# Kernel optimization log

Measured on AMD Instinct MI355X. Metric: run time of the kernel, lower is better.

Reference implementation:

```python
import jax, jax.numpy as jnp
import numpy as np

N_NODES = 1024
FEAT = 64
NEG_BIG = -9e15

def setup_inputs() -> dict:
    key = jax.random.key(0)
    ks = jax.random.split(key, 12)
    B, S, D = 4, 16384, FEAT
    flow_features = jax.random.normal(ks[0], (B, S, D), dtype=jnp.float32)
    src_ips = jax.random.randint(ks[1], (B, S), 0, N_NODES)
    dst_ips = jax.random.randint(ks[2], (B, S), 0, N_NODES)
    flow_volumes = jax.random.uniform(ks[3], (B, S), dtype=jnp.float32) * 2000.0
    emb = jax.random.normal(ks[4], (N_NODES, D), dtype=jnp.float32) * 0.02
    We1 = jax.random.normal(ks[5], (2 * D, 32), dtype=jnp.float32) * 0.1
    be1 = jnp.zeros((32,), dtype=jnp.float32)
    We2 = jax.random.normal(ks[6], (32, 1), dtype=jnp.float32) * 0.1
    be2 = jnp.zeros((1,), dtype=jnp.float32)
    W = jax.random.normal(ks[7], (D, D), dtype=jnp.float32) * 0.1
    a1 = jax.random.normal(ks[8], (D,), dtype=jnp.float32) * 0.1
    a2 = jax.random.normal(ks[9], (D,), dtype=jnp.float32) * 0.1
    return dict(flow_features=flow_features, src_ips=src_ips, dst_ips=dst_ips,
                flow_volumes=flow_volumes, emb=emb, We1=We1, be1=be1, We2=We2,
                be2=be2, W=W, a1=a1, a2=a2)

def _forward(flow_features, flow_volumes, emb, We1, be1, We2, be2, W, a1, a2,
             src_ips, dst_ips):
    B, S, D = flow_features.shape
    N = emb.shape[0]
    # --- DynamicGraphBuilder: scatter-add flow features at dst nodes ---
    node = jax.vmap(lambda f, d: jnp.zeros((N, D), f.dtype).at[d].add(f))(
        flow_features, dst_ips)                         # (B, N, D)
    nrm = jnp.maximum(jnp.linalg.norm(node, axis=-1, keepdims=True), 1e-12)
    h = node / nrm                                      # F.normalize(p=2)
    # --- edge weights: MLP over concat(src_emb, dst_emb), scaled by volume ---
    pair = jnp.concatenate([emb[src_ips], emb[dst_ips]], axis=-1)  # (B, S, 2D)
    mid = jax.nn.relu(pair @ We1 + be1)
    ew = jax.nn.sigmoid((mid @ We2 + be2)[..., 0])      # (B, S)
    w = ew * jax.nn.sigmoid(flow_volumes / 1000.0)
    adj = jax.vmap(lambda s, d, ww: jnp.zeros((N, N), ww.dtype)
                   .at[s, d].set(ww).at[d, s].set(ww))(src_ips, dst_ips, w)
    # --- GraphAttentionLayer (decomposed e_ij = a1.Wh_i + a2.Wh_j) ---
    Wh = h @ W                                          # (B, N, D)
    f1 = Wh @ a1                                        # (B, N)
    f2 = Wh @ a2                                        # (B, N)
    e = jax.nn.leaky_relu(f1[:, :, None] + f2[:, None, :], 0.2)  # (B, N, N)
    attn = jax.nn.softmax(jnp.where(adj > 0, e, NEG_BIG), axis=-1)
    return jax.nn.elu(jnp.einsum('bij,bjd->bid', attn, Wh))       # (B, N, D)

def reference(flow_features, src_ips, dst_ips, flow_volumes, emb, We1, be1,
              We2, be2, W, a1, a2):
    return _forward(flow_features, flow_volumes, emb, We1, be1, We2, be2,
                    W, a1, a2, src_ips, dst_ips)
```

## Files before the change

kernel.cpp:

```cpp
#include <hip/hip_runtime.h>
#include <math.h>

#define BB 4
#define SS 16384
#define NN 1024
#define DD 64
#define MW 32
#define KSEG 32
#define CAPSEG 12
#define NCAP 128

__device__ __forceinline__ float wave_sum(float v) {
    #pragma unroll
    for (int off = 32; off > 0; off >>= 1) v += __shfl_xor(v, off, 64);
    return v;
}
__device__ __forceinline__ float wave_max(float v) {
    #pragma unroll
    for (int off = 32; off > 0; off >>= 1) v = fmaxf(v, __shfl_xor(v, off, 64));
    return v;
}

__global__ __launch_bounds__(512) void build_kernel(
        const int* __restrict__ src_ips, const int* __restrict__ dst_ips,
        int* __restrict__ cnt_d_seg, int* __restrict__ cnt_s_seg,
        int* __restrict__ bkt_d, int* __restrict__ bkt_s) {
    __shared__ int cd[NN], cs_[NN];
    int t = threadIdx.x;
    cd[t] = 0; cd[t + 512] = 0; cs_[t] = 0; cs_[t + 512] = 0;
    __syncthreads();
    int b = blockIdx.x >> 5, seg = blockIdx.x & 31;
    int local = (seg << 9) + t;
    int f = (b << 14) + local;
    int src = src_ips[f], dst = dst_ips[f];
    int rowbase = blockIdx.x << 10;
    int pd = atomicAdd(&cd[dst], 1);
    if (pd < CAPSEG) bkt_d[(size_t)(rowbase + dst) * CAPSEG + pd] = local | (src << 16);
    int ps = atomicAdd(&cs_[src], 1);
    if (ps < CAPSEG) bkt_s[(size_t)(rowbase + src) * CAPSEG + ps] = dst;
    __syncthreads();
    cnt_d_seg[rowbase + t]       = min(cd[t], CAPSEG);
    cnt_d_seg[rowbase + t + 512] = min(cd[t + 512], CAPSEG);
    cnt_s_seg[rowbase + t]       = min(cs_[t], CAPSEG);
    cnt_s_seg[rowbase + t + 512] = min(cs_[t + 512], CAPSEG);
}

__global__ __launch_bounds__(256) void gather_kernel(
        const float* __restrict__ ff, const int* __restrict__ cnt_d_seg,
        const int* __restrict__ cnt_s_seg, const int* __restrict__ bkt_d,
        const int* __restrict__ bkt_s, const float* __restrict__ W,
        const float* __restrict__ a1, const float* __restrict__ a2,
        float* __restrict__ Wh, float* __restrict__ f1, float* __restrict__ f2,
        int* __restrict__ nbr, int* __restrict__ cntn) {
    __shared__ float Ws[DD * DD];
    __shared__ float hs[4][DD];
    __shared__ unsigned int bm[4][MW];
    __shared__ float a1s[DD], a2s[DD];
    int t = threadIdx.x, wave = t >> 6, lane = t & 63;
    for (int i = t; i < DD * DD / 4; i += 256)
        ((float4*)Ws)[i] = ((const float4*)W)[i];
    if (t < DD) { a1s[t] = a1[t]; a2s[t] = a2[t]; }
    int row = blockIdx.x * 4 + wave;
    int b = row >> 10, i = row & (NN - 1);
    if (lane < MW) bm[wave][lane] = 0u;

    int segbase = (b << 15) + i;
    int cv_d = (lane < KSEG) ? cnt_d_seg[segbase + (lane << 10)] : 0;
    int cv_s = (lane < KSEG) ? cnt_s_seg[segbase + (lane << 10)] : 0;
    int xd = cv_d, xs = cv_s;
    #pragma unroll
    for (int off = 1; off < 64; off <<= 1) {
        int yd = __shfl_up(xd, off, 64);
        int ys = __shfl_up(xs, off, 64);
        if (lane >= off) { xd += yd; xs += ys; }
    }
    int c1 = __shfl(xd, 63, 64);
    int c2 = __shfl(xs, 63, 64);
    int bd0 = xd - cv_d, bs0 = xs - cv_s;
    int bkreg = 0, dreg = 0;
    for (int s = 0; s < KSEG; ++s) {
        int csd = __shfl(cv_d, s, 64), bd = __shfl(bd0, s, 64);
        if (lane >= bd && lane < bd + csd)
            bkreg = bkt_d[(size_t)(segbase + (s << 10)) * CAPSEG + (lane - bd)];
        int css = __shfl(cv_s, s, 64), bs = __shfl(bs0, s, 64);
        if (lane >= bs && lane < bs + css)
            dreg = bkt_s[(size_t)(segbase + (s << 10)) * CAPSEG + (lane - bs)];
    }

    int fq = lane >> 4, qi = lane & 15;
    const float* ffb = ff + (size_t)b * SS * DD;
    float4 v0 = make_float4(0.f, 0.f, 0.f, 0.f);
    float4 v1 = make_float4(0.f, 0.f, 0.f, 0.f);
    int lim = min(c1, 64);
    for (int base = 0; base < lim; base += 8) {
        int w0 = __shfl(bkreg, base + fq, 64);
        int w1 = __shfl(bkreg, base + 4 + fq, 64);
        if (base + fq < lim) {
            float4 x = ((const float4*)(ffb + (size_t)(w0 & 0xFFFF) * DD))[qi];
            v0.x += x.x; v0.y += x.y; v0.z += x.z; v0.w += x.w;
        }
        if (base + 4 + fq < lim) {
            float4 x = ((const float4*)(ffb + (size_t)(w1 & 0xFFFF) * DD))[qi];
            v1.x += x.x; v1.y += x.y; v1.z += x.z; v1.w += x.w;
        }
    }
    float4 v = make_float4(v0.x + v1.x, v0.y + v1.y, v0.z + v1.z, v0.w + v1.w);
    #pragma unroll
    for (int off = 16; off <= 32; off <<= 1) {
        v.x += __shfl_xor(v.x, off, 64);
        v.y += __shfl_xor(v.y, off, 64);
        v.z += __shfl_xor(v.z, off, 64);
        v.w += __shfl_xor(v.w, off, 64);
    }
    float ssq = (fq == 0) ? (v.x*v.x + v.y*v.y + v.z*v.z + v.w*v.w) : 0.f;
    float nrm = fmaxf(sqrtf(wave_sum(ssq)), 1e-12f);
    float inv = 1.f / nrm;
    __syncthreads();
    if (fq == 0)
        ((float4*)hs[wave])[qi] = make_float4(v.x*inv, v.y*inv, v.z*inv, v.w*inv);
    float whl = 0.f;
    #pragma unroll
    for (int k = 0; k < DD; ++k)
        whl = fmaf(hs[wave][k], Ws[k * DD + lane], whl);
    Wh[(size_t)row * DD + lane] = whl;
    float p1 = wave_sum(whl * a1s[lane]);
    float p2 = wave_sum(whl * a2s[lane]);
    if (lane == 0) { f1[row] = p1; f2[row] = p2; }

    if (lane < lim) {
        int s = (bkreg >> 16) & 0x3FF;
        atomicOr(&bm[wave][s >> 5], 1u << (s & 31));
    }
    int lim2 = min(c2, 64);
    if (lane < lim2) {
        int d = dreg & 0x3FF;
        atomicOr(&bm[wave][d >> 5], 1u << (d & 31));
    }
    unsigned int mw_ = (lane < MW) ? bm[wave][lane] : 0u;
    int pc = __popc(mw_);
    int x = pc;
    #pragma unroll
    for (int off = 1; off < 64; off <<= 1) {
        int y = __shfl_up(x, off, 64);
        if (lane >= off) x += y;
    }
    int cnt = __shfl(x, 63, 64);
    int o = x - pc;
    int* nrow = nbr + (size_t)row * NCAP;
    unsigned int bits = mw_;
    while (bits) {
        int bi = __ffs(bits) - 1; bits &= bits - 1;
        nrow[o++] = (lane << 5) + bi;
    }
    if (lane == 0) cntn[row] = cnt;
}

__global__ __launch_bounds__(256) void attn_kernel(
        const int* __restrict__ cntn, const int* __restrict__ nbr,
        const float* __restrict__ f1, const float* __restrict__ f2,
        const float* __restrict__ Wh, float* __restrict__ out) {
    __shared__ int jls[4][NCAP];
    int t = threadIdx.x, wave = t >> 6, lane = t & 63;
    int row = blockIdx.x * 4 + wave;
    int b = row >> 10;
    int fq = lane >> 4, qi = lane & 15;
    int cnt = cntn[row];
    float f1i = f1[row];
    const float* f2b = f2 + b * NN;
    const float* Whb = Wh + (size_t)(b << 10) * DD;
    const int* nrow = nbr + (size_t)row * NCAP;
    for (int k = lane; k < cnt; k += 64) jls[wave][k] = nrow[k];

    if (cnt > 0) {
        float m = -INFINITY;
        for (int k = lane; k < cnt; k += 64) {
            float e = f1i + f2b[jls[wave][k]];
            e = (e >= 0.f) ? e : 0.2f * e;
            m = fmaxf(m, e);
        }
        m = wave_max(m);
        float4 a0 = make_float4(0.f, 0.f, 0.f, 0.f);
        float4 a1v = make_float4(0.f, 0.f, 0.f, 0.f);
        float psum = 0.f;
        for (int k = fq; k < cnt; k += 8) {
            int j0 = jls[wave][k];
            float e0 = f1i + f2b[j0];
            e0 = (e0 >= 0.f) ? e0 : 0.2f * e0;
            float p0 = __expf(e0 - m);
            float4 w0 = ((const float4*)(Whb + (size_t)j0 * DD))[qi];
            a0.x = fmaf(p0, w0.x, a0.x);
            a0.y = fmaf(p0, w0.y, a0.y);
            a0.z = fmaf(p0, w0.z, a0.z);
            a0.w = fmaf(p0, w0.w, a0.w);
            psum += p0;
            int k1 = k + 4;
            if (k1 < cnt) {
                int j1 = jls[wave][k1];
                float e1 = f1i + f2b[j1];
                e1 = (e1 >= 0.f) ? e1 : 0.2f * e1;
                float p1 = __expf(e1 - m);
                float4 w1 = ((const float4*)(Whb + (size_t)j1 * DD))[qi];
                a1v.x = fmaf(p1, w1.x, a1v.x);
                a1v.y = fmaf(p1, w1.y, a1v.y);
                a1v.z = fmaf(p1, w1.z, a1v.z);
                a1v.w = fmaf(p1, w1.w, a1v.w);
                psum += p1;
            }
        }
        float4 acc = make_float4(a0.x + a1v.x, a0.y + a1v.y,
                                 a0.z + a1v.z, a0.w + a1v.w);
        #pragma unroll
        for (int off = 16; off <= 32; off <<= 1) {
            acc.x += __shfl_xor(acc.x, off, 64);
            acc.y += __shfl_xor(acc.y, off, 64);
            acc.z += __shfl_xor(acc.z, off, 64);
            acc.w += __shfl_xor(acc.w, off, 64);
        }
        float lsum = wave_sum(psum) * (1.f / 16.f);
        if (fq == 0) {
            float invl = 1.f / lsum;
            float4 r;
            r.x = acc.x * invl; r.y = acc.y * invl;
            r.z = acc.z * invl; r.w = acc.w * invl;
            r.x = (r.x > 0.f) ? r.x : expm1f(r.x);
            r.y = (r.y > 0.f) ? r.y : expm1f(r.y);
            r.z = (r.z > 0.f) ? r.z : expm1f(r.z);
            r.w = (r.w > 0.f) ? r.w : expm1f(r.w);
            ((float4*)(out + (size_t)row * DD))[qi] = r;
        }
    } else {
        float4 acc = make_float4(0.f, 0.f, 0.f, 0.f);
        for (int k = fq; k < NN; k += 4) {
            float4 w = ((const float4*)(Whb + (size_t)k * DD))[qi];
            acc.x += w.x; acc.y += w.y; acc.z += w.z; acc.w += w.w;
        }
        #pragma unroll
        for (int off = 16; off <= 32; off <<= 1) {
            acc.x += __shfl_xor(acc.x, off, 64);
            acc.y += __shfl_xor(acc.y, off, 64);
            acc.z += __shfl_xor(acc.z, off, 64);
            acc.w += __shfl_xor(acc.w, off, 64);
        }
        if (fq == 0) {
            float4 r;
            r.x = acc.x * (1.f / NN); r.y = acc.y * (1.f / NN);
            r.z = acc.z * (1.f / NN); r.w = acc.w * (1.f / NN);
            r.x = (r.x > 0.f) ? r.x : expm1f(r.x);
            r.y = (r.y > 0.f) ? r.y : expm1f(r.y);
            r.z = (r.z > 0.f) ? r.z : expm1f(r.z);
            r.w = (r.w > 0.f) ? r.w : expm1f(r.w);
            ((float4*)(out + (size_t)row * DD))[qi] = r;
        }
    }
}

extern "C" void kernel_launch(void* const* d_in, const int* in_sizes, int n_in,
                              void* d_out, int out_size, void* d_ws, size_t ws_size,
                              hipStream_t stream) {
    const float* ff      = (const float*)d_in[0];
    const int*   src_ips = (const int*)d_in[1];
    const int*   dst_ips = (const int*)d_in[2];
    const float* W  = (const float*)d_in[9];
    const float* a1 = (const float*)d_in[10];
    const float* a2 = (const float*)d_in[11];
    float* out = (float*)d_out;

    char* ws = (char*)d_ws;
    int* cnt_d_seg = (int*)ws;
    int* cnt_s_seg = (int*)(ws + (512 << 10));
    int* bkt_d     = (int*)(ws + (1 << 20));
    int* bkt_s     = (int*)(ws + (7 << 20));
    float* Wh      = (float*)(ws + (13 << 20));
    float* f1      = (float*)(ws + (14 << 20));
    float* f2      = (float*)(ws + (14 << 20) + (16 << 10));
    int*   cntn    = (int*)(ws + (14 << 20) + (32 << 10));
    int*   nbr     = (int*)(ws + (15 << 20));

    build_kernel<<<BB * KSEG, 512, 0, stream>>>(src_ips, dst_ips,
                                                cnt_d_seg, cnt_s_seg, bkt_d, bkt_s);
    gather_kernel<<<BB * NN / 4, 256, 0, stream>>>(ff, cnt_d_seg, cnt_s_seg,
                                                   bkt_d, bkt_s, W, a1, a2,
                                                   Wh, f1, f2, nbr, cntn);
    attn_kernel<<<BB * NN / 4, 256, 0, stream>>>(cntn, nbr, f1, f2, Wh, out);
}
```

Before: 105.5 us.

## Pack bucket counts, transpose bucket layout, drop W smem staging, cache f2 in LDS

The build kernel now stores per-segment destination and source counts packed into one byte, and lays buckets out node-major (node, segment, slot) with 16-bit source buckets, so each gather wave reads contiguous memory instead of strided segments. The gather kernel drops the 16KB shared-memory copy of W and the a1/a2 staging plus a block barrier, reading W directly from global and cache. The packed counts need only one prefix scan. The attention kernel stages the batch's f2 vector in LDS, which adds a block-wide barrier and per-block load overhead.

Measured after the change: 102.6 us (median of 2 runs). -2.8%, faster.

```diff
diff --git a/kernel.cpp b/kernel.cpp
--- a/kernel.cpp
+++ b/kernel.cpp
@@ -23,8 +23,8 @@
 
 __global__ __launch_bounds__(512) void build_kernel(
         const int* __restrict__ src_ips, const int* __restrict__ dst_ips,
-        int* __restrict__ cnt_d_seg, int* __restrict__ cnt_s_seg,
-        int* __restrict__ bkt_d, int* __restrict__ bkt_s) {
+        unsigned char* __restrict__ cnt8, int* __restrict__ bkt_d,
+        unsigned short* __restrict__ bkt_s) {
     __shared__ int cd[NN], cs_[NN];
     int t = threadIdx.x;
     cd[t] = 0; cd[t + 512] = 0; cs_[t] = 0; cs_[t + 512] = 0;
@@ -33,58 +33,58 @@
     int local = (seg << 9) + t;
     int f = (b << 14) + local;
     int src = src_ips[f], dst = dst_ips[f];
-    int rowbase = blockIdx.x << 10;
     int pd = atomicAdd(&cd[dst], 1);
-    if (pd < CAPSEG) bkt_d[(size_t)(rowbase + dst) * CAPSEG + pd] = local | (src << 16);
+    if (pd < CAPSEG)
+        bkt_d[(size_t)(((b << 10) + dst) * KSEG + seg) * CAPSEG + pd]
+            = local | (src << 16);
     int ps = atomicAdd(&cs_[src], 1);
-    if (ps < CAPSEG) bkt_s[(size_t)(rowbase + src) * CAPSEG + ps] = dst;
+    if (ps < CAPSEG)
+        bkt_s[(size_t)(((b << 10) + src) * KSEG + seg) * CAPSEG + ps]
+            = (unsigned short)dst;
     __syncthreads();
-    cnt_d_seg[rowbase + t]       = min(cd[t], CAPSEG);
-    cnt_d_seg[rowbase + t + 512] = min(cd[t + 512], CAPSEG);
-    cnt_s_seg[rowbase + t]       = min(cs_[t], CAPSEG);
-    cnt_s_seg[rowbase + t + 512] = min(cs_[t + 512], CAPSEG);
+    int n0 = t, n1 = t + 512;
+    cnt8[(size_t)((b << 10) + n0) * KSEG + seg]
+        = (unsigned char)(min(cd[n0], CAPSEG) | (min(cs_[n0], CAPSEG) << 4));
+    cnt8[(size_t)((b << 10) + n1) * KSEG + seg]
+        = (unsigned char)(min(cd[n1], CAPSEG) | (min(cs_[n1], CAPSEG) << 4));
 }
 
 __global__ __launch_bounds__(256) void gather_kernel(
-        const float* __restrict__ ff, const int* __restrict__ cnt_d_seg,
-        const int* __restrict__ cnt_s_seg, const int* __restrict__ bkt_d,
-        const int* __restrict__ bkt_s, const float* __restrict__ W,
-        const float* __restrict__ a1, const float* __restrict__ a2,
-        float* __restrict__ Wh, float* __restrict__ f1, float* __restrict__ f2,
+        const float* __restrict__ ff, const unsigned char* __restrict__ cnt8,
+        const int* __restrict__ bkt_d, const unsigned short* __restrict__ bkt_s,
+        const float* __restrict__ W, const float* __restrict__ a1,
+        const float* __restrict__ a2, float* __restrict__ Wh,
+        float* __restrict__ f1, float* __restrict__ f2,
         int* __restrict__ nbr, int* __restrict__ cntn) {
-    __shared__ float Ws[DD * DD];
     __shared__ float hs[4][DD];
     __shared__ unsigned int bm[4][MW];
-    __shared__ float a1s[DD], a2s[DD];
     int t = threadIdx.x, wave = t >> 6, lane = t & 63;
-    for (int i = t; i < DD * DD / 4; i += 256)
-        ((float4*)Ws)[i] = ((const float4*)W)[i];
-    if (t < DD) { a1s[t] = a1[t]; a2s[t] = a2[t]; }
     int row = blockIdx.x * 4 + wave;
-    int b = row >> 10, i = row & (NN - 1);
+    int b = row >> 10;
     if (lane < MW) bm[wave][lane] = 0u;
 
-    int segbase = (b << 15) + i;
-    int cv_d = (lane < KSEG) ? cnt_d_seg[segbase + (lane << 10)] : 0;
-    int cv_s = (lane < KSEG) ? cnt_s_seg[segbase + (lane << 10)] : 0;
-    int xd = cv_d, xs = cv_s;
+    int cb = (lane < KSEG) ? (int)cnt8[(size_t)row * KSEG + lane] : 0;
+    int cv = (cb & 15) | ((cb >> 4) << 16);
+    int x = cv;
     #pragma unroll
     for (int off = 1; off < 64; off <<= 1) {
-        int yd = __shfl_up(xd, off, 64);
-        int ys = __shfl_up(xs, off, 64);
-        if (lane >= off) { xd += yd; xs += ys; }
-    }
-    int c1 = __shfl(xd, 63, 64);
-    int c2 = __shfl(xs, 63, 64);
-    int bd0 = xd - cv_d, bs0 = xs - cv_s;
-    int bkreg = 0, dreg = 0;
+        int y = __shfl_up(x, off, 64);
+        if (lane >= off) x += y;
+    }
+    int tot = __shfl(x, 63, 64);
+    int c1 = tot & 0xFFFF, c2 = tot >> 16;
+    int ex = x - cv;
+    int bkreg = 0, dreg = -1;
+    size_t rowB = (size_t)row * (KSEG * CAPSEG);
     for (int s = 0; s < KSEG; ++s) {
-        int csd = __shfl(cv_d, s, 64), bd = __shfl(bd0, s, 64);
+        int cvs = __shfl(cv, s, 64);
+        int exs = __shfl(ex, s, 64);
+        int csd = cvs & 0xFFFF, bd = exs & 0xFFFF;
+        int css = cvs >> 16,    bs = exs >> 16;
         if (lane >= bd && lane < bd + csd)
-            bkreg = bkt_d[(size_t)(segbase + (s << 10)) * CAPSEG + (lane - bd)];
-        int css = __shfl(cv_s, s, 64), bs = __shfl(bs0, s, 64);
+            bkreg = bkt_d[rowB + s * CAPSEG + (lane - bd)];
         if (lane >= bs && lane < bs + css)
-            dreg = bkt_s[(size_t)(segbase + (s << 10)) * CAPSEG + (lane - bs)];
+            dreg = bkt_s[rowB + s * CAPSEG + (lane - bs)];
     }
 
     int fq = lane >> 4, qi = lane & 15;
@@ -96,12 +96,12 @@
         int w0 = __shfl(bkreg, base + fq, 64);
         int w1 = __shfl(bkreg, base + 4 + fq, 64);
         if (base + fq < lim) {
-            float4 x = ((const float4*)(ffb + (size_t)(w0 & 0xFFFF) * DD))[qi];
-            v0.x += x.x; v0.y += x.y; v0.z += x.z; v0.w += x.w;
+            float4 xv = ((const float4*)(ffb + (size_t)(w0 & 0xFFFF) * DD))[qi];
+            v0.x += xv.x; v0.y += xv.y; v0.z += xv.z; v0.w += xv.w;
         }
         if (base + 4 + fq < lim) {
-            float4 x = ((const float4*)(ffb + (size_t)(w1 & 0xFFFF) * DD))[qi];
-            v1.x += x.x; v1.y += x.y; v1.z += x.z; v1.w += x.w;
+            float4 xv = ((const float4*)(ffb + (size_t)(w1 & 0xFFFF) * DD))[qi];
+            v1.x += xv.x; v1.y += xv.y; v1.z += xv.z; v1.w += xv.w;
         }
     }
     float4 v = make_float4(v0.x + v1.x, v0.y + v1.y, v0.z + v1.z, v0.w + v1.w);
@@ -115,37 +115,35 @@
     float ssq = (fq == 0) ? (v.x*v.x + v.y*v.y + v.z*v.z + v.w*v.w) : 0.f;
     float nrm = fmaxf(sqrtf(wave_sum(ssq)), 1e-12f);
     float inv = 1.f / nrm;
-    __syncthreads();
     if (fq == 0)
         ((float4*)hs[wave])[qi] = make_float4(v.x*inv, v.y*inv, v.z*inv, v.w*inv);
     float whl = 0.f;
-    #pragma unroll
+    #pragma unroll 8
     for (int k = 0; k < DD; ++k)
-        whl = fmaf(hs[wave][k], Ws[k * DD + lane], whl);
+        whl = fmaf(hs[wave][k], W[k * DD + lane], whl);
     Wh[(size_t)row * DD + lane] = whl;
-    float p1 = wave_sum(whl * a1s[lane]);
-    float p2 = wave_sum(whl * a2s[lane]);
+    float p1 = wave_sum(whl * a1[lane]);
+    float p2 = wave_sum(whl * a2[lane]);
     if (lane == 0) { f1[row] = p1; f2[row] = p2; }
 
     if (lane < lim) {
         int s = (bkreg >> 16) & 0x3FF;
         atomicOr(&bm[wave][s >> 5], 1u << (s & 31));
     }
-    int lim2 = min(c2, 64);
-    if (lane < lim2) {
+    if (dreg >= 0) {
         int d = dreg & 0x3FF;
         atomicOr(&bm[wave][d >> 5], 1u << (d & 31));
     }
     unsigned int mw_ = (lane < MW) ? bm[wave][lane] : 0u;
     int pc = __popc(mw_);
-    int x = pc;
+    int xc = pc;
     #pragma unroll
     for (int off = 1; off < 64; off <<= 1) {
-        int y = __shfl_up(x, off, 64);
-        if (lane >= off) x += y;
-    }
-    int cnt = __shfl(x, 63, 64);
-    int o = x - pc;
+        int y = __shfl_up(xc, off, 64);
+        if (lane >= off) xc += y;
+    }
+    int cnt = __shfl(xc, 63, 64);
+    int o = xc - pc;
     int* nrow = nbr + (size_t)row * NCAP;
     unsigned int bits = mw_;
     while (bits) {
@@ -159,22 +157,24 @@
         const int* __restrict__ cntn, const int* __restrict__ nbr,
         const float* __restrict__ f1, const float* __restrict__ f2,
         const float* __restrict__ Wh, float* __restrict__ out) {
+    __shared__ float f2s[NN];
     __shared__ int jls[4][NCAP];
     int t = threadIdx.x, wave = t >> 6, lane = t & 63;
     int row = blockIdx.x * 4 + wave;
     int b = row >> 10;
+    for (int k = t; k < NN; k += 256) f2s[k] = f2[b * NN + k];
     int fq = lane >> 4, qi = lane & 15;
     int cnt = cntn[row];
     float f1i = f1[row];
-    const float* f2b = f2 + b * NN;
     const float* Whb = Wh + (size_t)(b << 10) * DD;
     const int* nrow = nbr + (size_t)row * NCAP;
     for (int k = lane; k < cnt; k += 64) jls[wave][k] = nrow[k];
+    __syncthreads();
 
     if (cnt > 0) {
         float m = -INFINITY;
         for (int k = lane; k < cnt; k += 64) {
-            float e = f1i + f2b[jls[wave][k]];
+            float e = f1i + f2s[jls[wave][k]];
             e = (e >= 0.f) ? e : 0.2f * e;
             m = fmaxf(m, e);
         }
@@ -184,7 +184,7 @@
         float psum = 0.f;
         for (int k = fq; k < cnt; k += 8) {
             int j0 = jls[wave][k];
-            float e0 = f1i + f2b[j0];
+            float e0 = f1i + f2s[j0];
             e0 = (e0 >= 0.f) ? e0 : 0.2f * e0;
             float p0 = __expf(e0 - m);
             float4 w0 = ((const float4*)(Whb + (size_t)j0 * DD))[qi];
@@ -196,7 +196,7 @@
             int k1 = k + 4;
             if (k1 < cnt) {
                 int j1 = jls[wave][k1];
-                float e1 = f1i + f2b[j1];
+                float e1 = f1i + f2s[j1];
                 e1 = (e1 >= 0.f) ? e1 : 0.2f * e1;
                 float p1 = __expf(e1 - m);
                 float4 w1 = ((const float4*)(Whb + (size_t)j1 * DD))[qi];
@@ -266,20 +266,19 @@
     float* out = (float*)d_out;
 
     char* ws = (char*)d_ws;
-    int* cnt_d_seg = (int*)ws;
-    int* cnt_s_seg = (int*)(ws + (512 << 10));
-    int* bkt_d     = (int*)(ws + (1 << 20));
-    int* bkt_s     = (int*)(ws + (7 << 20));
-    float* Wh      = (float*)(ws + (13 << 20));
-    float* f1      = (float*)(ws + (14 << 20));
-    float* f2      = (float*)(ws + (14 << 20) + (16 << 10));
-    int*   cntn    = (int*)(ws + (14 << 20) + (32 << 10));
-    int*   nbr     = (int*)(ws + (15 << 20));
+    unsigned char* cnt8   = (unsigned char*)ws;
+    int*           bkt_d  = (int*)(ws + (1 << 20));
+    unsigned short* bkt_s = (unsigned short*)(ws + (8 << 20));
+    float* Wh   = (float*)(ws + (12 << 20));
+    float* f1   = (float*)(ws + (13 << 20));
+    float* f2   = (float*)(ws + (13 << 20) + (16 << 10));
+    int*   cntn = (int*)(ws + (13 << 20) + (32 << 10));
+    int*   nbr  = (int*)(ws + (14 << 20));
 
     build_kernel<<<BB * KSEG, 512, 0, stream>>>(src_ips, dst_ips,
-                                                cnt_d_seg, cnt_s_seg, bkt_d, bkt_s);
-    gather_kernel<<<BB * NN / 4, 256, 0, stream>>>(ff, cnt_d_seg, cnt_s_seg,
-                                                   bkt_d, bkt_s, W, a1, a2,
-                                                   Wh, f1, f2, nbr, cntn);
+                                                cnt8, bkt_d, bkt_s);
+    gather_kernel<<<BB * NN / 4, 256, 0, stream>>>(ff, cnt8, bkt_d, bkt_s,
+                                                   W, a1, a2, Wh, f1, f2,
+                                                   nbr, cntn);
     attn_kernel<<<BB * NN / 4, 256, 0, stream>>>(cntn, nbr, f1, f2, Wh, out);
 }
```
